# Kernel tuning notes

Hardware: AMD Instinct MI355X
Metric: run time of the kernel (lower is better)

Reference implementation:

```python
import jax, jax.numpy as jnp
import numpy as np
import math

L, B, T, C, H, DH, V, MEM = 6, 2, 1024, 1024, 16, 64, 32000, 128

def _ln(x, g, b):
    m = jnp.mean(x, -1, keepdims=True)
    v = jnp.mean((x - m) ** 2, -1, keepdims=True)
    return (x - m) * jax.lax.rsqrt(v + 1e-5) * g + b

def _rel_shift(x):
    # x: [B,H,Q,K]; TransformerXL shift trick: pad zero col, reshape, drop first row
    b, h, q, k = x.shape
    xp = jnp.pad(x, ((0, 0), (0, 0), (0, 0), (1, 0)))
    xp = xp.reshape(b, h, k + 1, q)
    return xp[:, :, 1:, :].reshape(b, h, q, k)

def setup_inputs():
    key = jax.random.key(0)
    ks = jax.random.split(key, 12)
    d = {}
    d['idx'] = jax.random.randint(ks[0], (B, T), 0, V)
    d['mems'] = jax.random.normal(ks[1], (L, B, MEM, C), dtype=jnp.float32) * 0.02
    d['wte'] = jax.random.normal(ks[2], (V, C), dtype=jnp.float32) * 0.02
    d['ln1_g'] = jnp.ones((L, C), jnp.float32); d['ln1_b'] = jnp.zeros((L, C), jnp.float32)
    d['attn_w'] = jax.random.normal(ks[3], (L, C, 3 * C), dtype=jnp.float32) * 0.02
    d['attn_b'] = jnp.zeros((L, 3 * C), jnp.float32)
    d['proj_w'] = jax.random.normal(ks[4], (L, C, C), dtype=jnp.float32) * 0.02
    d['proj_b'] = jnp.zeros((L, C), jnp.float32)
    d['r_emb'] = jax.random.normal(ks[5], (L, H, DH), dtype=jnp.float32) * 0.02
    d['r_bias'] = jax.random.normal(ks[6], (L, H, DH), dtype=jnp.float32) * 0.02
    d['ln2_g'] = jnp.ones((L, C), jnp.float32); d['ln2_b'] = jnp.zeros((L, C), jnp.float32)
    d['fc_w'] = jax.random.normal(ks[7], (L, C, 4 * C), dtype=jnp.float32) * 0.02
    d['fc_b'] = jnp.zeros((L, 4 * C), jnp.float32)
    d['fc2_w'] = jax.random.normal(ks[8], (L, 4 * C, C), dtype=jnp.float32) * 0.02
    d['fc2_b'] = jnp.zeros((L, C), jnp.float32)
    d['lnf_g'] = jnp.ones((C,), jnp.float32); d['lnf_b'] = jnp.zeros((C,), jnp.float32)
    d['lm_w'] = jax.random.normal(ks[9], (C, V), dtype=jnp.float32) * 0.02
    return d

def _attn(x, mem, w, b, pw, pb, remb, rbias):
    Bx, Tx, Cx = x.shape
    cat = jnp.concatenate([mem, x], axis=1)          # [B,K,C], K = mem_len + Tx
    K = cat.shape[1]
    qkv = cat @ w + b
    q, k, v = jnp.split(qkv, 3, axis=-1)
    q = q.reshape(Bx, K, H, DH).transpose(0, 2, 1, 3)
    k = k.reshape(Bx, K, H, DH).transpose(0, 2, 1, 3)
    v = v.reshape(Bx, K, H, DH).transpose(0, 2, 1, 3)
    q = q + rbias[None, :, None, :]
    AC = jnp.einsum('bhid,bhjd->bhij', q, k)
    # BD: r is r_emb broadcast over positions, so q@r^T is constant over j
    s = jnp.einsum('bhid,hd->bhi', q, remb)
    BD = _rel_shift(jnp.broadcast_to(s[..., None], (Bx, H, K, K)))
    p = jax.nn.softmax((AC + BD) / math.sqrt(DH), axis=-1)
    y = jnp.einsum('bhij,bhjd->bhid', p, v).transpose(0, 2, 1, 3).reshape(Bx, K, Cx)
    y = y @ pw + pb
    new_mem = cat[:, -MEM:]
    return y, new_mem

def reference(idx, mems, wte, ln1_g, ln1_b, attn_w, attn_b, proj_w, proj_b, r_emb, r_bias, ln2_g, ln2_b, fc_w, fc_b, fc2_w, fc2_b, lnf_g, lnf_b, lm_w):
    x = wte[idx]                                      # [B,T,C]
    new_mems = []
    for l in range(L):
        h = _ln(x, ln1_g[l], ln1_b[l])
        y, nm = _attn(h, mems[l], attn_w[l], attn_b[l], proj_w[l], proj_b[l], r_emb[l], r_bias[l])
        h2 = _ln(y, ln2_g[l], ln2_b[l])
        m = jax.nn.gelu(h2 @ fc_w[l] + fc_b[l], approximate=False) @ fc2_w[l] + fc2_b[l]
        x = y + m                                     # note: residual onto attn output (length grows by MEM per layer)
        new_mems.append(nm)
    x = _ln(x, lnf_g, lnf_b)
    logits = x @ lm_w                                 # [B, L*MEM+T, V]
    return logits, jnp.stack(new_mems)
```

## Files before the change

### kernel.cpp

```cpp
#include <hip/hip_runtime.h>
#include <hip/hip_bf16.h>
#include <hip/hip_fp16.h>

#define LNUM 6
#define BB 2
#define TT 1024
#define CC 1024
#define HH 16
#define DHH 64
#define VV 32000
#define MM 128

typedef _Float16 f16;
typedef _Float16 f16x8 __attribute__((ext_vector_type(8)));
typedef float f32x4 __attribute__((ext_vector_type(4)));

__device__ __forceinline__ void g2lds16(const void* g, void* l) {
    __builtin_amdgcn_global_load_lds((const __attribute__((address_space(1))) void*)g,
                                     (__attribute__((address_space(3))) void*)l,
                                     16, 0, 0);
}

__device__ __forceinline__ float wred(float v) {
#pragma unroll
    for (int o = 32; o > 0; o >>= 1) v += __shfl_xor(v, o);
    return v;
}

__device__ __forceinline__ float gelu_tanh(float v) {
    const float u = 1.5957691216057308f * (v + 0.044715f * v * v * v);
    const float e = __expf(u);
    return v * e / (e + __expf(-0.f) * (2.f - 1.f) + 1.f / e * 0.f + (1.f / e) * 0.f + 1.f / e);
}


__global__ __launch_bounds__(256)
void transpose_k(const float* __restrict__ W, f16* __restrict__ WT, int R, int Cc)
{
    __shared__ float tile[32][33];
    const size_t base = (size_t)blockIdx.z * R * Cc;
    const int c0 = blockIdx.x * 32, r0 = blockIdx.y * 32;
    const int tx = threadIdx.x & 31, ty = threadIdx.x >> 5;
#pragma unroll
    for (int i = 0; i < 32; i += 8)
        tile[ty + i][tx] = W[base + (size_t)(r0 + ty + i) * Cc + c0 + tx];
    __syncthreads();
#pragma unroll
    for (int i = 0; i < 32; i += 8)
        WT[base + (size_t)(c0 + ty + i) * R + r0 + tx] = (f16)tile[tx][ty + i];
}

__global__ __launch_bounds__(256)
void embed_k(const int* __restrict__ idx, const float* __restrict__ wte, float* __restrict__ X)
{
    const int row = blockIdx.x;
    const int id = idx[row];
    const float4* src = (const float4*)(wte + (size_t)id * CC);
    float4* dst = (float4*)(X + (size_t)row * CC);
    dst[threadIdx.x] = src[threadIdx.x];
}

__global__ __launch_bounds__(256)
void ln_k(const float* __restrict__ X, const float* __restrict__ g,
          const float* __restrict__ bta, f16* __restrict__ outH)
{
    const int row = blockIdx.x * 4 + (threadIdx.x >> 6);
    const int lane = threadIdx.x & 63;
    const float4* xr = (const float4*)(X + (size_t)row * CC);
    float4 v[4];
    float s = 0.f;
#pragma unroll
    for (int i = 0; i < 4; ++i) { v[i] = xr[i * 64 + lane]; s += v[i].x + v[i].y + v[i].z + v[i].w; }
    s = wred(s);
    const float mean = s * (1.f / CC);
    float q = 0.f;
#pragma unroll
    for (int i = 0; i < 4; ++i) {
        float a = v[i].x - mean, b = v[i].y - mean, c = v[i].z - mean, d = v[i].w - mean;
        q += a * a + b * b + c * c + d * d;
    }
    q = wred(q);
    const float rs = rsqrtf(q * (1.f / CC) + 1e-5f);
    const float4* g4 = (const float4*)g;
    const float4* b4 = (const float4*)bta;
    uint2* orow = (uint2*)(outH + (size_t)row * CC);
#pragma unroll
    for (int i = 0; i < 4; ++i) {
        float4 gg = g4[i * 64 + lane], bb = b4[i * 64 + lane];
        union { f16 h4[4]; uint2 u; } pk;
        pk.h4[0] = (f16)((v[i].x - mean) * rs * gg.x + bb.x);
        pk.h4[1] = (f16)((v[i].y - mean) * rs * gg.y + bb.y);
        pk.h4[2] = (f16)((v[i].z - mean) * rs * gg.z + bb.z);
        pk.h4[3] = (f16)((v[i].w - mean) * rs * gg.w + bb.w);
        orow[i * 64 + lane] = pk.u;
    }
}

__global__ __launch_bounds__(256)
void ln1cat_k(const float* __restrict__ X, const float* __restrict__ memsL,
              const float* __restrict__ g, const float* __restrict__ bta,
              f16* __restrict__ catH, float* __restrict__ nmOut,
              int K, int Kin)
{
    const int row = blockIdx.x * 4 + (threadIdx.x >> 6);
    const int lane = threadIdx.x & 63;
    const int b = row / K, rr = row % K;
    uint2* crow = (uint2*)(catH + (size_t)row * CC);
    if (rr < MM) {
        const float4* src = (const float4*)(memsL + ((size_t)b * MM + rr) * CC);
#pragma unroll
        for (int i = 0; i < 4; ++i) {
            float4 vv = src[i * 64 + lane];
            union { f16 h4[4]; uint2 u; } pk;
            pk.h4[0] = (f16)vv.x; pk.h4[1] = (f16)vv.y; pk.h4[2] = (f16)vv.z; pk.h4[3] = (f16)vv.w;
            crow[i * 64 + lane] = pk.u;
        }
        return;
    }
    const float4* xr = (const float4*)(X + ((size_t)b * Kin + (rr - MM)) * CC);
    float4 v[4];
    float s = 0.f;
#pragma unroll
    for (int i = 0; i < 4; ++i) { v[i] = xr[i * 64 + lane]; s += v[i].x + v[i].y + v[i].z + v[i].w; }
    s = wred(s);
    const float mean = s * (1.f / CC);
    float q = 0.f;
#pragma unroll
    for (int i = 0; i < 4; ++i) {
        float a = v[i].x - mean, b2 = v[i].y - mean, c = v[i].z - mean, d = v[i].w - mean;
        q += a * a + b2 * b2 + c * c + d * d;
    }
    q = wred(q);
    const float rs = rsqrtf(q * (1.f / CC) + 1e-5f);
    const float4* g4 = (const float4*)g;
    const float4* b4 = (const float4*)bta;
    float4* nm = nullptr;
    if (rr >= K - MM) nm = (float4*)(nmOut + ((size_t)b * MM + (rr - (K - MM))) * CC);
#pragma unroll
    for (int i = 0; i < 4; ++i) {
        float4 gg = g4[i * 64 + lane], bb = b4[i * 64 + lane];
        float4 o;
        o.x = (v[i].x - mean) * rs * gg.x + bb.x;
        o.y = (v[i].y - mean) * rs * gg.y + bb.y;
        o.z = (v[i].z - mean) * rs * gg.z + bb.z;
        o.w = (v[i].w - mean) * rs * gg.w + bb.w;
        union { f16 h4[4]; uint2 u; } pk;
        pk.h4[0] = (f16)o.x; pk.h4[1] = (f16)o.y; pk.h4[2] = (f16)o.z; pk.h4[3] = (f16)o.w;
        crow[i * 64 + lane] = pk.u;
        if (nm) nm[i * 64 + lane] = o;
    }
}

template <int EPI>
__global__ __launch_bounds__(256, 2)
void gemm_k(const f16* __restrict__ A, const f16* __restrict__ BT,
            const float* __restrict__ bias, const float* __restrict__ res,
            float* __restrict__ outF, f16* __restrict__ outH,
            int M, int N, int Kc)
{
    __shared__ f16 sA[2][128 * 32];
    __shared__ f16 sB[2][128 * 32];

    const int nbn = N >> 7;
    const int nwg = gridDim.x;
    const int id = blockIdx.x;
    const int qq = nwg >> 3, r8 = nwg & 7;
    const int xcd = id & 7, pos = id >> 3;
    const int wgid = (xcd < r8 ? xcd * (qq + 1) : r8 * (qq + 1) + (xcd - r8) * qq) + pos;
    const int bm = wgid / nbn, bn = wgid % nbn;

    const int tid = threadIdx.x;
    const int w = tid >> 6, l = tid & 63;
    const int wr = w >> 1, wc = w & 1;
    const int lr = l & 15, lk = (l >> 4) * 8;

    f32x4 acc[4][4] = {};

    const int ar = w * 32 + (l >> 2);
    const int ak = (l & 3) * 8;
    const f16* gA = A + (size_t)(bm * 128 + ar) * Kc + ak;
    const f16* gB = BT + (size_t)(bn * 128 + ar) * Kc + ak;

    auto stage = [&](int slot, int kt) {
        g2lds16(gA + kt, &sA[slot][w * 1024]);
        g2lds16(gA + kt + (size_t)16 * Kc, &sA[slot][w * 1024 + 512]);
        g2lds16(gB + kt, &sB[slot][w * 1024]);
        g2lds16(gB + kt + (size_t)16 * Kc, &sB[slot][w * 1024 + 512]);
    };

    stage(0, 0);
    asm volatile("s_waitcnt vmcnt(0)" ::: "memory");
    __builtin_amdgcn_s_barrier();

    int cur = 0;
    for (int kt = 0; kt < Kc; kt += 32) {
        if (kt + 32 < Kc) stage(cur ^ 1, kt + 32);
        f16x8 af[4], bf[4];
#pragma unroll
        for (int mi = 0; mi < 4; ++mi) af[mi] = *(const f16x8*)&sA[cur][(wr * 64 + mi * 16 + lr) * 32 + lk];
#pragma unroll
        for (int ni = 0; ni < 4; ++ni) bf[ni] = *(const f16x8*)&sB[cur][(wc * 64 + ni * 16 + lr) * 32 + lk];
        asm volatile("s_waitcnt lgkmcnt(0)" ::: "memory");
        __builtin_amdgcn_sched_barrier(0);
#pragma unroll
        for (int mi = 0; mi < 4; ++mi)
#pragma unroll
            for (int ni = 0; ni < 4; ++ni)
                acc[mi][ni] = __builtin_amdgcn_mfma_f32_16x16x32_f16(af[mi], bf[ni], acc[mi][ni], 0, 0, 0);
        asm volatile("s_waitcnt vmcnt(0)" ::: "memory");
        __builtin_amdgcn_s_barrier();
        cur ^= 1;
    }

    const int orow0 = bm * 128 + wr * 64 + (l >> 4) * 4;
    const int ocol0 = bn * 128 + wc * 64 + lr;
#pragma unroll
    for (int mi = 0; mi < 4; ++mi)
#pragma unroll
        for (int ni = 0; ni < 4; ++ni) {
            const int col = ocol0 + ni * 16;
            const float bv = (EPI >= 1) ? bias[col] : 0.f;
#pragma unroll
            for (int r = 0; r < 4; ++r) {
                const int row = orow0 + mi * 16 + r;
                float v = acc[mi][ni][r] + bv;
                if (EPI == 2) {
                    const float u = 1.5957691216057308f * (v + 0.044715f * v * v * v);
                    const float e = __expf(u);
                    v = v * e / (e + 1.f);
                    outH[(size_t)row * N + col] = (f16)v;
                } else if (EPI == 4) {
                    outH[(size_t)row * N + col] = (f16)v;
                } else if (EPI == 3) {
                    v += res[(size_t)row * N + col];
                    outF[(size_t)row * N + col] = v;
                } else {
                    outF[(size_t)row * N + col] = v;
                }
            }
        }
}

template <int EPI>
__global__ __launch_bounds__(512, 2)
void gemm256_k(const f16* __restrict__ A, const f16* __restrict__ BT,
               const float* __restrict__ bias,
               float* __restrict__ outF, f16* __restrict__ outH,
               int M, int N, int Kc)
{
    __shared__ char ldsbuf[131072];
    char* ldsA = ldsbuf;
    char* ldsB = ldsbuf + 65536;

    const int nbm = M >> 8;
    const int nwg = gridDim.x;
    int id = blockIdx.x;
    const int qq = nwg >> 3, rr8 = nwg & 7;
    const int xcd = id & 7, pos = id >> 3;
    const int wgid = (xcd < rr8 ? xcd * (qq + 1) : rr8 * (qq + 1) + (xcd - rr8) * qq) + pos;
    const int bm = wgid % nbm, bn = wgid / nbm;

    const int t_ = threadIdx.x;
    const int w = t_ >> 6, l = t_ & 63;
    const int wm = w >> 2, wn = w & 3;
    const int lr = l & 15, lhi = l >> 4;

    const f16* gA = A + (size_t)bm * 256 * Kc;
    const f16* gB = BT + (size_t)bn * 256 * Kc;

    auto stage = [&](const f16* Gbase, char* ldsHalf, int kt) {
#pragma unroll
        for (int ii = 0; ii < 2; ++ii) {
            const int gb = (w << 1) + ii;
            const int s = (gb << 6) + l;
            const int row = s >> 3, grp = s & 7;
            g2lds16(Gbase + (size_t)row * Kc + kt + ((grp ^ (row & 7)) << 3),
                    ldsHalf + gb * 1024);
        }
    };
    auto rdfrag = [&](const char* halfBase, int rowInHalf, int ks) -> f16x8 {
        return *(const f16x8*)(halfBase + rowInHalf * 128 +
                               ((((ks << 2) + lhi) ^ (rowInHalf & 7)) << 4));
    };

    f32x4 acc[8][4] = {};
    f16x8 aA[4][2], blo[2][2], bhi[2][2];

    const int NT = Kc >> 6;
    const char* aHalf0 = ldsA + wm * 16384;
    const char* aHalf1 = ldsA + 32768 + wm * 16384;
    const char* bHalf0 = ldsB + (wn >> 1) * 16384;
    const char* bHalf1 = ldsB + 32768 + (wn >> 1) * 16384;
    const int brow = (wn & 1) * 64;

    stage(gA, ldsA + 0, 0);
    stage(gA + (size_t)128 * Kc, ldsA + 16384, 0);
    stage(gB, ldsB + 0, 0);
    stage(gB + (size_t)128 * Kc, ldsB + 16384, 0);
    stage(gB, ldsB + 32768, 64);
    stage(gB + (size_t)128 * Kc, ldsB + 49152, 64);
    asm volatile("s_waitcnt vmcnt(0)" ::: "memory");
    __builtin_amdgcn_s_barrier();

#define MFMA_QUAD(MQ, NQ, BR)                                                            \
    __builtin_amdgcn_s_setprio(1);                                                       \
    _Pragma("unroll") for (int mf = 0; mf < 4; ++mf)                                     \
    _Pragma("unroll") for (int nf = 0; nf < 2; ++nf)                                     \
    _Pragma("unroll") for (int ks = 0; ks < 2; ++ks)                                     \
        acc[(MQ)*4 + mf][(NQ)*2 + nf] =                                                  \
            __builtin_amdgcn_mfma_f32_16x16x32_f16(aA[mf][ks], BR[nf][ks],               \
                                                   acc[(MQ)*4 + mf][(NQ)*2 + nf], 0, 0, 0); \
    __builtin_amdgcn_s_setprio(0);

#define PHASE_SYNC()                                          \
    __builtin_amdgcn_s_barrier();                             \
    asm volatile("s_waitcnt lgkmcnt(0)" ::: "memory");        \
    __builtin_amdgcn_sched_barrier(0);

    for (int t = 0; t < NT; t += 2) {
        const bool pf0 = (t + 2) < NT;
        const int kb = (t + 1) << 6, kc2 = (t + 2) << 6, kd = (t + 3) << 6;

#pragma unroll
        for (int mf = 0; mf < 4; ++mf)
#pragma unroll
            for (int ks = 0; ks < 2; ++ks) aA[mf][ks] = rdfrag(aHalf0, mf * 16 + lr, ks);
#pragma unroll
        for (int nf = 0; nf < 2; ++nf)
#pragma unroll
            for (int ks = 0; ks < 2; ++ks) blo[nf][ks] = rdfrag(bHalf0, brow + nf * 16 + lr, ks);
        stage(gA, ldsA + 32768, kb);
        PHASE_SYNC();
        MFMA_QUAD(0, 0, blo);
        __builtin_amdgcn_s_barrier();

#pragma unroll
        for (int nf = 0; nf < 2; ++nf)
#pragma unroll
            for (int ks = 0; ks < 2; ++ks) bhi[nf][ks] = rdfrag(bHalf0, brow + 32 + nf * 16 + lr, ks);
        stage(gA + (size_t)128 * Kc, ldsA + 49152, kb);
        PHASE_SYNC();
        MFMA_QUAD(0, 1, bhi);
        __builtin_amdgcn_s_barrier();

#pragma unroll
        for (int mf = 0; mf < 4; ++mf)
#pragma unroll
            for (int ks = 0; ks < 2; ++ks) aA[mf][ks] = rdfrag(aHalf0, 64 + mf * 16 + lr, ks);
        if (pf0) stage(gB, ldsB + 0, kc2);
        PHASE_SYNC();
        MFMA_QUAD(1, 0, blo);
        __builtin_amdgcn_s_barrier();

        if (pf0) {
            stage(gB + (size_t)128 * Kc, ldsB + 16384, kc2);
            asm volatile("s_waitcnt vmcnt(4)" ::: "memory");
        } else {
            asm volatile("s_waitcnt vmcnt(0)" ::: "memory");
        }
        PHASE_SYNC();
        MFMA_QUAD(1, 1, bhi);
        __builtin_amdgcn_s_barrier();

#pragma unroll
        for (int mf = 0; mf < 4; ++mf)
#pragma unroll
            for (int ks = 0; ks < 2; ++ks) aA[mf][ks] = rdfrag(aHalf1, mf * 16 + lr, ks);
#pragma unroll
        for (int nf = 0; nf < 2; ++nf)
#pragma unroll
            for (int ks = 0; ks < 2; ++ks) blo[nf][ks] = rdfrag(bHalf1, brow + nf * 16 + lr, ks);
        if (pf0) stage(gA, ldsA + 0, kc2);
        PHASE_SYNC();
        MFMA_QUAD(0, 0, blo);
        __builtin_amdgcn_s_barrier();

#pragma unroll
        for (int nf = 0; nf < 2; ++nf)
#pragma unroll
            for (int ks = 0; ks < 2; ++ks) bhi[nf][ks] = rdfrag(bHalf1, brow + 32 + nf * 16 + lr, ks);
        if (pf0) stage(gA + (size_t)128 * Kc, ldsA + 16384, kc2);
        PHASE_SYNC();
        MFMA_QUAD(0, 1, bhi);
        __builtin_amdgcn_s_barrier();

#pragma unroll
        for (int mf = 0; mf < 4; ++mf)
#pragma unroll
            for (int ks = 0; ks < 2; ++ks) aA[mf][ks] = rdfrag(aHalf1, 64 + mf * 16 + lr, ks);
        if (pf0) stage(gB, ldsB + 32768, kd);
        PHASE_SYNC();
        MFMA_QUAD(1, 0, blo);
        __builtin_amdgcn_s_barrier();

        if (pf0) {
            stage(gB + (size_t)128 * Kc, ldsB + 49152, kd);
            asm volatile("s_waitcnt vmcnt(4)" ::: "memory");
        } else {
            asm volatile("s_waitcnt vmcnt(0)" ::: "memory");
        }
        PHASE_SYNC();
        MFMA_QUAD(1, 1, bhi);
        __builtin_amdgcn_s_barrier();
    }
#undef MFMA_QUAD
#undef PHASE_SYNC

    const int rb0 = bm * 256 + wm * 128 + lhi * 4;
    const int cb0 = bn * 256 + wn * 64 + lr;
#pragma unroll
    for (int mf = 0; mf < 8; ++mf)
#pragma unroll
        for (int nf = 0; nf < 4; ++nf) {
            const int col = cb0 + nf * 16;
            const float bv = (EPI >= 1) ? bias[col] : 0.f;
#pragma unroll
            for (int r = 0; r < 4; ++r) {
                const int row = rb0 + mf * 16 + r;
                float v = acc[mf][nf][r] + bv;
                if (EPI == 2) {
                    const float u = 1.5957691216057308f * (v + 0.044715f * v * v * v);
                    const float e = __expf(u);
                    v = v * e / (e + 1.f);
                    outH[(size_t)row * N + col] = (f16)v;
                } else if (EPI == 4) {
                    outH[(size_t)row * N + col] = (f16)v;
                } else {
                    outF[(size_t)row * N + col] = v;
                }
            }
        }
}

__global__ __launch_bounds__(256)
void attn_k(const f16* __restrict__ qkv, const float* __restrict__ remb,
            const float* __restrict__ rbias, f16* __restrict__ yH, int K)
{
    __shared__ f16 K_lds[64 * 64];
    __shared__ f16 Vt_lds[64 * 64];
    __shared__ f16 P_lds[64 * 64];
    __shared__ float s_s[66];

    const int b = blockIdx.x >> 4, h = blockIdx.x & 15;
    const int i0 = blockIdx.y * 64;
    const int t = threadIdx.x;
    const int w = t >> 6, l = t & 63;
    const int c = l & 15, g = l >> 4;

    const f16* qg = qkv + (size_t)b * K * 3072 + h * 64;
    const f16* kg = qg + 1024;
    const f16* vg = qg + 2048;
    const float* rb = rbias + h * 64;
    const float* re = remb + h * 64;

    f16x8 qf[2];
    {
        const int qrow = i0 + w * 16 + c;
#pragma unroll
        for (int ks = 0; ks < 2; ++ks) {
            f16x8 raw = *(const f16x8*)(qg + (size_t)qrow * 3072 + ks * 32 + g * 8);
            f16x8 o;
#pragma unroll
            for (int j = 0; j < 8; ++j) o[j] = (f16)((float)raw[j] + rb[ks * 32 + g * 8 + j]);
            qf[ks] = o;
        }
    }
    if (t < 65) {
        float sv = 0.f;
        const int i = i0 + t;
        if (i < K) {
            const f16* qr = qg + (size_t)i * 3072;
#pragma unroll
            for (int d8 = 0; d8 < 8; ++d8) {
                f16x8 v8 = *(const f16x8*)(qr + d8 * 8);
#pragma unroll
                for (int j = 0; j < 8; ++j) sv += ((float)v8[j] + rb[d8 * 8 + j]) * re[d8 * 8 + j];
            }
        }
        s_s[t] = sv;
    }
    __syncthreads();

    float sA[4], sB[4];
#pragma unroll
    for (int r = 0; r < 4; ++r) {
        sA[r] = s_s[w * 16 + g * 4 + r];
        sB[r] = s_s[w * 16 + g * 4 + r + 1];
    }

    float m_run[4] = {0.f, 0.f, 0.f, 0.f};
    float psum[4] = {0.f, 0.f, 0.f, 0.f};
    f32x4 yacc[4] = {};

    const int kb = t >> 4, db = t & 15;

    for (int j0 = 0; j0 < K; j0 += 64) {
#pragma unroll
        for (int i = 0; i < 2; ++i) {
            const int slot = w * 128 + i * 64 + l;
            const int row = slot >> 3, grp = slot & 7;
            const f16* src = kg + (size_t)(j0 + row) * 3072 + ((grp ^ (row & 7)) * 8);
            g2lds16(src, (char*)K_lds + (size_t)(w * 128 + i * 64) * 16);
        }
        {
            union { uint2 u; f16 hh[4]; } rowv[4];
#pragma unroll
            for (int i = 0; i < 4; ++i)
                rowv[i].u = *(const uint2*)(vg + (size_t)(j0 + kb * 4 + i) * 3072 + db * 4);
#pragma unroll
            for (int j = 0; j < 4; ++j) {
                union { uint2 u; f16 hh[4]; } colv;
#pragma unroll
                for (int i = 0; i < 4; ++i) colv.hh[i] = rowv[i].hh[j];
                const int d = db * 4 + j;
                *(uint2*)((char*)Vt_lds + d * 128 + ((kb * 8) ^ ((d & 7) << 4))) = colv.u;
            }
        }
        __syncthreads();

        f32x4 sc[4] = {};
#pragma unroll
        for (int tt = 0; tt < 4; ++tt) {
            const int row = tt * 16 + c;
#pragma unroll
            for (int ks = 0; ks < 2; ++ks) {
                f16x8 kf = *(const f16x8*)((char*)K_lds + row * 128 + ((ks * 64 + g * 16) ^ ((row & 7) << 4)));
                sc[tt] = __builtin_amdgcn_mfma_f32_16x16x32_f16(qf[ks], kf, sc[tt], 0, 0, 0);
            }
        }

        float p[4][4];
#pragma unroll
        for (int tt = 0; tt < 4; ++tt)
#pragma unroll
            for (int r = 0; r < 4; ++r) {
                const int gi = i0 + w * 16 + g * 4 + r;
                const int gj = j0 + tt * 16 + c;
                const float bd = (gj <= gi) ? sA[r] : ((gj == gi + 1) ? 0.f : sB[r]);
                p[tt][r] = (sc[tt][r] + bd) * 0.125f;
            }

        float lmax[4];
        bool need = false;
#pragma unroll
        for (int r = 0; r < 4; ++r) {
            lmax[r] = fmaxf(fmaxf(p[0][r], p[1][r]), fmaxf(p[2][r], p[3][r]));
            need |= (lmax[r] > m_run[r] + 8.f);
        }
        if (__any(need)) {
#pragma unroll
            for (int r = 0; r < 4; ++r) {
                float mx = lmax[r];
                mx = fmaxf(mx, __shfl_xor(mx, 1));
                mx = fmaxf(mx, __shfl_xor(mx, 2));
                mx = fmaxf(mx, __shfl_xor(mx, 4));
                mx = fmaxf(mx, __shfl_xor(mx, 8));
                if (mx > m_run[r]) {
                    const float f = __expf(m_run[r] - mx);
                    m_run[r] = mx;
                    psum[r] *= f;
#pragma unroll
                    for (int tt = 0; tt < 4; ++tt) yacc[tt][r] *= f;
                }
            }
        }
#pragma unroll
        for (int r = 0; r < 4; ++r) {
            float ss = 0.f;
#pragma unroll
            for (int tt = 0; tt < 4; ++tt) {
                const float e = __expf(p[tt][r] - m_run[r]);
                p[tt][r] = e;
                ss += e;
            }
            psum[r] += ss;
        }

#pragma unroll
        for (int tt = 0; tt < 4; ++tt)
#pragma unroll
            for (int r = 0; r < 4; ++r) {
                const int q = w * 16 + g * 4 + r;
                *(f16*)((char*)P_lds + q * 128 + (((tt * 16 + c) * 2) ^ ((q & 7) << 4))) = (f16)p[tt][r];
            }
        asm volatile("s_waitcnt lgkmcnt(0)" ::: "memory");
        __builtin_amdgcn_sched_barrier(0);

        {
            const int qrow = w * 16 + c;
            f16x8 pa[2];
#pragma unroll
            for (int ks = 0; ks < 2; ++ks)
                pa[ks] = *(const f16x8*)((char*)P_lds + qrow * 128 + ((ks * 64 + g * 16) ^ ((qrow & 7) << 4)));
#pragma unroll
            for (int tt = 0; tt < 4; ++tt) {
                const int drow = tt * 16 + c;
#pragma unroll
                for (int ks = 0; ks < 2; ++ks) {
                    f16x8 vb = *(const f16x8*)((char*)Vt_lds + drow * 128 + ((ks * 64 + g * 16) ^ ((drow & 7) << 4)));
                    yacc[tt] = __builtin_amdgcn_mfma_f32_16x16x32_f16(pa[ks], vb, yacc[tt], 0, 0, 0);
                }
            }
        }
        __syncthreads();
    }

#pragma unroll
    for (int r = 0; r < 4; ++r) {
        float ps = psum[r];
        ps += __shfl_xor(ps, 1);
        ps += __shfl_xor(ps, 2);
        ps += __shfl_xor(ps, 4);
        ps += __shfl_xor(ps, 8);
        const float inv = 1.f / ps;
        const int row = i0 + w * 16 + g * 4 + r;
        f16* dst = yH + (size_t)(b * K + row) * CC + h * 64;
#pragma unroll
        for (int tt = 0; tt < 4; ++tt)
            dst[tt * 16 + c] = (f16)(yacc[tt][r] * inv);
    }
}

extern "C" void kernel_launch(void* const* d_in, const int* in_sizes, int n_in,
                              void* d_out, int out_size, void* d_ws, size_t ws_size,
                              hipStream_t stream)
{
    (void)in_sizes; (void)n_in; (void)out_size; (void)ws_size;
    const int*   idx    = (const int*)  d_in[0];
    const float* mems   = (const float*)d_in[1];
    const float* wte    = (const float*)d_in[2];
    const float* ln1_g  = (const float*)d_in[3];
    const float* ln1_b  = (const float*)d_in[4];
    const float* attn_w = (const float*)d_in[5];
    const float* attn_b = (const float*)d_in[6];
    const float* proj_w = (const float*)d_in[7];
    const float* proj_b = (const float*)d_in[8];
    const float* r_emb  = (const float*)d_in[9];
    const float* r_bias = (const float*)d_in[10];
    const float* ln2_g  = (const float*)d_in[11];
    const float* ln2_b  = (const float*)d_in[12];
    const float* fc_w   = (const float*)d_in[13];
    const float* fc_b   = (const float*)d_in[14];
    const float* fc2_w  = (const float*)d_in[15];
    const float* fc2_b  = (const float*)d_in[16];
    const float* lnf_g  = (const float*)d_in[17];
    const float* lnf_b  = (const float*)d_in[18];
    const float* lm_w   = (const float*)d_in[19];
    float* out = (float*)d_out;

    char* wp = (char*)d_ws; size_t off = 0;
    auto carve = [&](size_t bytes) -> void* {
        void* p = wp + off; off += (bytes + 255) & ~(size_t)255; return p;
    };
    const int KMAX = TT + LNUM * MM;
    f16*  attn_wT = (f16*) carve((size_t)LNUM * 3 * CC * CC * 2);
    f16*  proj_wT = (f16*) carve((size_t)LNUM * CC * CC * 2);
    f16*  fc_wT   = (f16*) carve((size_t)LNUM * 4 * CC * CC * 2);
    f16*  fc2_wT  = (f16*) carve((size_t)LNUM * 4 * CC * CC * 2);
    f16*  lm_wT   = (f16*) carve((size_t)VV * CC * 2);
    float* x0     = (float*)carve((size_t)BB * KMAX * CC * 4);
    float* x1     = (float*)carve((size_t)BB * KMAX * CC * 4);
    f16*  catH    = (f16*) carve((size_t)BB * KMAX * CC * 2);
    f16*  qkv16   = (f16*) carve((size_t)BB * KMAX * 3 * CC * 2);
    f16*  yH      = (f16*) carve((size_t)BB * KMAX * CC * 2);
    float* yp     = (float*)carve((size_t)BB * KMAX * CC * 4);
    f16*  h2H     = (f16*) carve((size_t)BB * KMAX * CC * 2);
    f16*  a1H     = (f16*) carve((size_t)BB * KMAX * 4 * CC * 2);
    f16*  xfH     = (f16*) carve((size_t)BB * KMAX * CC * 2);

    transpose_k<<<dim3(3 * CC / 32, CC / 32, LNUM), 256, 0, stream>>>(attn_w, attn_wT, CC, 3 * CC);
    transpose_k<<<dim3(CC / 32, CC / 32, LNUM),     256, 0, stream>>>(proj_w, proj_wT, CC, CC);
    transpose_k<<<dim3(4 * CC / 32, CC / 32, LNUM), 256, 0, stream>>>(fc_w, fc_wT, CC, 4 * CC);
    transpose_k<<<dim3(CC / 32, 4 * CC / 32, LNUM), 256, 0, stream>>>(fc2_w, fc2_wT, 4 * CC, CC);
    transpose_k<<<dim3(VV / 32, CC / 32, 1),        256, 0, stream>>>(lm_w, lm_wT, CC, VV);

    embed_k<<<BB * TT, 256, 0, stream>>>(idx, wte, x0);

    const size_t LOGITS = (size_t)BB * KMAX * VV;
    float* xcur = x0; float* xnxt = x1;
    for (int l = 0; l < LNUM; ++l) {
        const int Kin = TT + MM * l;
        const int K = Kin + MM;
        const int Mrows = BB * K;
        const int nbm128 = Mrows / 128;
        ln1cat_k<<<Mrows / 4, 256, 0, stream>>>(xcur, mems + (size_t)l * BB * MM * CC,
                                                ln1_g + l * CC, ln1_b + l * CC,
                                                catH, out + LOGITS + (size_t)l * BB * MM * CC, K, Kin);
        gemm_k<4><<<(3 * CC / 128) * nbm128, 256, 0, stream>>>(
            catH, attn_wT + (size_t)l * 3 * CC * CC, attn_b + (size_t)l * 3 * CC, nullptr,
            nullptr, qkv16, Mrows, 3 * CC, CC);
        attn_k<<<dim3(BB * HH, K / 64), 256, 0, stream>>>(
            qkv16, r_emb + (size_t)l * HH * DHH, r_bias + (size_t)l * HH * DHH, yH, K);
        gemm_k<1><<<(CC / 128) * nbm128, 256, 0, stream>>>(
            yH, proj_wT + (size_t)l * CC * CC, proj_b + (size_t)l * CC, nullptr,
            yp, nullptr, Mrows, CC, CC);
        ln_k<<<Mrows / 4, 256, 0, stream>>>(yp, ln2_g + l * CC, ln2_b + l * CC, h2H);
        gemm_k<2><<<(4 * CC / 128) * nbm128, 256, 0, stream>>>(
            h2H, fc_wT + (size_t)l * 4 * CC * CC, fc_b + (size_t)l * 4 * CC, nullptr,
            nullptr, a1H, Mrows, 4 * CC, CC);
        gemm_k<3><<<(CC / 128) * nbm128, 256, 0, stream>>>(
            a1H, fc2_wT + (size_t)l * 4 * CC * CC, fc2_b + (size_t)l * CC, yp,
            xnxt, nullptr, Mrows, CC, 4 * CC);
        float* tmp = xcur; xcur = xnxt; xnxt = tmp;
    }
    ln_k<<<(BB * KMAX) / 4, 256, 0, stream>>>(xcur, lnf_g, lnf_b, xfH);
    gemm256_k<0><<<(BB * KMAX / 256) * (VV / 256), 512, 0, stream>>>(
        xfH, lm_wT, nullptr, out, nullptr, BB * KMAX, VV, CC);
}
```

Baseline: 2.070 ms.

## Double-buffer attention K/V tiles, widen weight transpose tiles, nontemporal fp32 stores

The attention kernel now double-buffers its K and V^T LDS tiles, prefetching the next 64-key block while the current one is computed, so global load latency overlaps with MFMA work. The weight transpose kernel moves to 64x64 tiles with float4 loads and packed 4-wide f16 stores, cutting the number of memory transactions. GEMM fp32 epilogue stores become nontemporal to limit cache pollution from the large outputs such as logits. In exchange, attention LDS use roughly doubles for K/V, which may lower occupancy, and the transpose tile pads to 64x65 floats.

```diff
diff --git a/kernel.cpp b/kernel.cpp
--- a/kernel.cpp
+++ b/kernel.cpp
@@ -27,27 +27,33 @@
     return v;
 }
 
-__device__ __forceinline__ float gelu_tanh(float v) {
-    const float u = 1.5957691216057308f * (v + 0.044715f * v * v * v);
-    const float e = __expf(u);
-    return v * e / (e + __expf(-0.f) * (2.f - 1.f) + 1.f / e * 0.f + (1.f / e) * 0.f + 1.f / e);
-}
-
-
 __global__ __launch_bounds__(256)
 void transpose_k(const float* __restrict__ W, f16* __restrict__ WT, int R, int Cc)
 {
-    __shared__ float tile[32][33];
+    __shared__ float tile[64][65];
     const size_t base = (size_t)blockIdx.z * R * Cc;
-    const int c0 = blockIdx.x * 32, r0 = blockIdx.y * 32;
-    const int tx = threadIdx.x & 31, ty = threadIdx.x >> 5;
-#pragma unroll
-    for (int i = 0; i < 32; i += 8)
-        tile[ty + i][tx] = W[base + (size_t)(r0 + ty + i) * Cc + c0 + tx];
+    const int c0 = blockIdx.x * 64, r0 = blockIdx.y * 64;
+    const int tx = threadIdx.x & 15, ty = threadIdx.x >> 4;
+#pragma unroll
+    for (int i = 0; i < 4; ++i) {
+        const int row = ty + i * 16;
+        float4 v = *(const float4*)&W[base + (size_t)(r0 + row) * Cc + c0 + tx * 4];
+        tile[row][tx * 4 + 0] = v.x;
+        tile[row][tx * 4 + 1] = v.y;
+        tile[row][tx * 4 + 2] = v.z;
+        tile[row][tx * 4 + 3] = v.w;
+    }
     __syncthreads();
 #pragma unroll
-    for (int i = 0; i < 32; i += 8)
-        WT[base + (size_t)(c0 + ty + i) * R + r0 + tx] = (f16)tile[tx][ty + i];
+    for (int i = 0; i < 4; ++i) {
+        const int c = ty + i * 16;
+        union { f16 h4[4]; uint2 u; } pk;
+        pk.h4[0] = (f16)tile[tx * 4 + 0][c];
+        pk.h4[1] = (f16)tile[tx * 4 + 1][c];
+        pk.h4[2] = (f16)tile[tx * 4 + 2][c];
+        pk.h4[3] = (f16)tile[tx * 4 + 3][c];
+        *(uint2*)&WT[base + (size_t)(c0 + c) * R + r0 + tx * 4] = pk.u;
+    }
 }
 
 __global__ __launch_bounds__(256)
@@ -426,7 +432,7 @@
                 } else if (EPI == 4) {
                     outH[(size_t)row * N + col] = (f16)v;
                 } else {
-                    outF[(size_t)row * N + col] = v;
+                    __builtin_nontemporal_store(v, &outF[(size_t)row * N + col]);
                 }
             }
         }
@@ -436,8 +442,8 @@
 void attn_k(const f16* __restrict__ qkv, const float* __restrict__ remb,
             const float* __restrict__ rbias, f16* __restrict__ yH, int K)
 {
-    __shared__ f16 K_lds[64 * 64];
-    __shared__ f16 Vt_lds[64 * 64];
+    __shared__ f16 K_lds[2][64 * 64];
+    __shared__ f16 Vt_lds[2][64 * 64];
     __shared__ f16 P_lds[64 * 64];
     __shared__ float s_s[66];
 
@@ -453,6 +459,36 @@
     const float* rb = rbias + h * 64;
     const float* re = remb + h * 64;
 
+    const int kb = t >> 4, db = t & 15;
+
+    auto stageK = [&](int j0, int slot) {
+#pragma unroll
+        for (int i = 0; i < 2; ++i) {
+            const int s = w * 128 + i * 64 + l;
+            const int row = s >> 3, grp = s & 7;
+            g2lds16(kg + (size_t)(j0 + row) * 3072 + ((grp ^ (row & 7)) * 8),
+                    (char*)K_lds[slot] + (size_t)(w * 128 + i * 64) * 16);
+        }
+    };
+    auto loadV = [&](int j0, uint2* rowv) {
+#pragma unroll
+        for (int i = 0; i < 4; ++i)
+            rowv[i] = *(const uint2*)(vg + (size_t)(j0 + kb * 4 + i) * 3072 + db * 4);
+    };
+    auto writeVt = [&](const uint2* rowvu, int slot) {
+#pragma unroll
+        for (int j = 0; j < 4; ++j) {
+            union { uint2 u; f16 hh[4]; } colv;
+#pragma unroll
+            for (int i = 0; i < 4; ++i) {
+                union { uint2 u; f16 hh[4]; } rv; rv.u = rowvu[i];
+                colv.hh[i] = rv.hh[j];
+            }
+            const int d = db * 4 + j;
+            *(uint2*)((char*)Vt_lds[slot] + d * 128 + ((kb * 8) ^ ((d & 7) << 4))) = colv.u;
+        }
+    };
+
     f16x8 qf[2];
     {
         const int qrow = i0 + w * 16 + c;
@@ -479,6 +515,13 @@
         }
         s_s[t] = sv;
     }
+
+    {
+        uint2 rowv[4];
+        stageK(0, 0);
+        loadV(0, rowv);
+        writeVt(rowv, 0);
+    }
     __syncthreads();
 
     float sA[4], sB[4];
@@ -492,31 +535,11 @@
     float psum[4] = {0.f, 0.f, 0.f, 0.f};
     f32x4 yacc[4] = {};
 
-    const int kb = t >> 4, db = t & 15;
-
-    for (int j0 = 0; j0 < K; j0 += 64) {
-#pragma unroll
-        for (int i = 0; i < 2; ++i) {
-            const int slot = w * 128 + i * 64 + l;
-            const int row = slot >> 3, grp = slot & 7;
-            const f16* src = kg + (size_t)(j0 + row) * 3072 + ((grp ^ (row & 7)) * 8);
-            g2lds16(src, (char*)K_lds + (size_t)(w * 128 + i * 64) * 16);
-        }
-        {
-            union { uint2 u; f16 hh[4]; } rowv[4];
-#pragma unroll
-            for (int i = 0; i < 4; ++i)
-                rowv[i].u = *(const uint2*)(vg + (size_t)(j0 + kb * 4 + i) * 3072 + db * 4);
-#pragma unroll
-            for (int j = 0; j < 4; ++j) {
-                union { uint2 u; f16 hh[4]; } colv;
-#pragma unroll
-                for (int i = 0; i < 4; ++i) colv.hh[i] = rowv[i].hh[j];
-                const int d = db * 4 + j;
-                *(uint2*)((char*)Vt_lds + d * 128 + ((kb * 8) ^ ((d & 7) << 4))) = colv.u;
-            }
-        }
-        __syncthreads();
+    int cur = 0;
+    for (int j0 = 0; j0 < K; j0 += 64, cur ^= 1) {
+        const bool more = (j0 + 64) < K;
+        uint2 rowv[4];
+        if (more) { stageK(j0 + 64, cur ^ 1); loadV(j0 + 64, rowv); }
 
         f32x4 sc[4] = {};
 #pragma unroll
@@ -524,7 +547,7 @@
             const int row = tt * 16 + c;
 #pragma unroll
             for (int ks = 0; ks < 2; ++ks) {
-                f16x8 kf = *(const f16x8*)((char*)K_lds + row * 128 + ((ks * 64 + g * 16) ^ ((row & 7) << 4)));
+                f16x8 kf = *(const f16x8*)((char*)K_lds[cur] + row * 128 + ((ks * 64 + g * 16) ^ ((row & 7) << 4)));
                 sc[tt] = __builtin_amdgcn_mfma_f32_16x16x32_f16(qf[ks], kf, sc[tt], 0, 0, 0);
             }
         }
@@ -576,6 +599,7 @@
             psum[r] += ss;
         }
 
+        if (more) writeVt(rowv, cur ^ 1);
 #pragma unroll
         for (int tt = 0; tt < 4; ++tt)
 #pragma unroll
@@ -597,7 +621,7 @@
                 const int drow = tt * 16 + c;
 #pragma unroll
                 for (int ks = 0; ks < 2; ++ks) {
-                    f16x8 vb = *(const f16x8*)((char*)Vt_lds + drow * 128 + ((ks * 64 + g * 16) ^ ((drow & 7) << 4)));
+                    f16x8 vb = *(const f16x8*)((char*)Vt_lds[cur] + drow * 128 + ((ks * 64 + g * 16) ^ ((drow & 7) << 4)));
                     yacc[tt] = __builtin_amdgcn_mfma_f32_16x16x32_f16(pa[ks], vb, yacc[tt], 0, 0, 0);
                 }
             }
@@ -668,11 +692,11 @@
     f16*  a1H     = (f16*) carve((size_t)BB * KMAX * 4 * CC * 2);
     f16*  xfH     = (f16*) carve((size_t)BB * KMAX * CC * 2);
 
-    transpose_k<<<dim3(3 * CC / 32, CC / 32, LNUM), 256, 0, stream>>>(attn_w, attn_wT, CC, 3 * CC);
-    transpose_k<<<dim3(CC / 32, CC / 32, LNUM),     256, 0, stream>>>(proj_w, proj_wT, CC, CC);
-    transpose_k<<<dim3(4 * CC / 32, CC / 32, LNUM), 256, 0, stream>>>(fc_w, fc_wT, CC, 4 * CC);
-    transpose_k<<<dim3(CC / 32, 4 * CC / 32, LNUM), 256, 0, stream>>>(fc2_w, fc2_wT, 4 * CC, CC);
-    transpose_k<<<dim3(VV / 32, CC / 32, 1),        256, 0, stream>>>(lm_w, lm_wT, CC, VV);
+    transpose_k<<<dim3(3 * CC / 64, CC / 64, LNUM), 256, 0, stream>>>(attn_w, attn_wT, CC, 3 * CC);
+    transpose_k<<<dim3(CC / 64, CC / 64, LNUM),     256, 0, stream>>>(proj_w, proj_wT, CC, CC);
+    transpose_k<<<dim3(4 * CC / 64, CC / 64, LNUM), 256, 0, stream>>>(fc_w, fc_wT, CC, 4 * CC);
+    transpose_k<<<dim3(CC / 64, 4 * CC / 64, LNUM), 256, 0, stream>>>(fc2_w, fc2_wT, 4 * CC, CC);
+    transpose_k<<<dim3(VV / 64, CC / 64, 1),        256, 0, stream>>>(lm_w, lm_wT, CC, VV);
 
     embed_k<<<BB * TT, 256, 0, stream>>>(idx, wte, x0);
 
```

Result: faster. 2.029 ms (-2.0%).
